# Kernel tuning notes

Hardware: AMD Instinct MI355X
Metric: run time of the kernel (lower is better)

## Reference

```python
import jax, jax.numpy as jnp
import numpy as np

B, T, I, H = 1024, 2048, 2, 64


def setup_inputs() -> dict:
    key = jax.random.key(0)
    k1, k2, k3 = jax.random.split(key, 3)
    x = jax.random.normal(k1, (B, T, I), dtype=jnp.float32)
    # Linear weights, torch nn.Linear layout: [out_features, in_features]
    W_h = jax.random.normal(k2, (H, H), dtype=jnp.float32) * (1.0 / np.sqrt(H))
    W_x = jax.random.normal(k3, (H, I), dtype=jnp.float32) * (1.0 / np.sqrt(I))
    return {"x": x, "W_h": W_h, "W_x": W_x}


def reference(x, W_h, W_x):
    # Manual ReLU RNN: h_{t} = relu(h_{t-1} @ W_h^T + x_t @ W_x^T), h_{-1} = 0
    Bx = x.shape[0]
    Hd = W_h.shape[0]
    h0 = jnp.zeros((Bx, Hd), dtype=x.dtype)
    # Precompute all input projections in one GEMM: [T, B, H]
    xin = jnp.einsum('bti,hi->tbh', x, W_x)

    def step(h, xt):
        h = jax.nn.relu(h @ W_h.T + xt)
        return h, None

    hT, _ = jax.lax.scan(step, h0, xin)
    # outputnn=False, hidden_size>1 -> L2 norm of final hidden state over hidden dim
    return jnp.linalg.norm(hT, axis=-1)  # [B]
```

## Files before the change

kernel.cpp:

```cpp
#include <hip/hip_runtime.h>
#include <math.h>

#define BB 1024
#define TT 2048
#define II 2
#define HH 64

#define PKF(A0,A1,B0,B1,W0,W1) \
 "v_pk_fma_f32 v[" A0 ":" A1 "], v[" B0 ":" B1 "], v[" W0 ":" W1 "], v[" A0 ":" A1 "]\n\t"
#define PKM(A0,A1,B0,B1,W0,W1) \
 "v_pk_mul_f32 v[" A0 ":" A1 "], v[" B0 ":" B1 "], v[" W0 ":" W1 "]\n\t"

#define RD16 \
 "ds_read_b128 v[128:131], v88\n\t" \
 "ds_read_b128 v[132:135], v88 offset:16\n\t" \
 "ds_read_b128 v[136:139], v88 offset:32\n\t" \
 "ds_read_b128 v[140:143], v88 offset:48\n\t" \
 "ds_read_b128 v[144:147], v88 offset:64\n\t" \
 "ds_read_b128 v[148:151], v88 offset:80\n\t" \
 "ds_read_b128 v[152:155], v88 offset:96\n\t" \
 "ds_read_b128 v[156:159], v88 offset:112\n\t" \
 "ds_read_b128 v[160:163], v88 offset:128\n\t" \
 "ds_read_b128 v[164:167], v88 offset:144\n\t" \
 "ds_read_b128 v[168:171], v88 offset:160\n\t" \
 "ds_read_b128 v[172:175], v88 offset:176\n\t" \
 "ds_read_b128 v[176:179], v88 offset:192\n\t" \
 "ds_read_b128 v[180:183], v88 offset:208\n\t" \
 "ds_read_b128 v[184:187], v88 offset:224\n\t" \
 "ds_read_b128 v[188:191], v88 offset:240\n\t"

#define PK_0_7 \
 "v_pk_fma_f32 v[76:77], v[128:129], v[12:13], v[92:93]\n\t" \
 PKM("78","79","130","131","14","15") \
 PKM("80","81","132","133","16","17") \
 PKM("82","83","134","135","18","19") \
 PKF("76","77","136","137","20","21") \
 PKF("78","79","138","139","22","23") \
 PKF("80","81","140","141","24","25") \
 PKF("82","83","142","143","26","27")
#define PK_8_15 \
 PKF("76","77","144","145","28","29") \
 PKF("78","79","146","147","30","31") \
 PKF("80","81","148","149","32","33") \
 PKF("82","83","150","151","34","35") \
 PKF("76","77","152","153","36","37") \
 PKF("78","79","154","155","38","39") \
 PKF("80","81","156","157","40","41") \
 PKF("82","83","158","159","42","43")
#define PK_16_23 \
 PKF("76","77","160","161","44","45") \
 PKF("78","79","162","163","46","47") \
 PKF("80","81","164","165","48","49") \
 PKF("82","83","166","167","50","51") \
 PKF("76","77","168","169","52","53") \
 PKF("78","79","170","171","54","55") \
 PKF("80","81","172","173","56","57") \
 PKF("82","83","174","175","58","59")
#define PK_24_31 \
 PKF("76","77","176","177","60","61") \
 PKF("78","79","178","179","62","63") \
 PKF("80","81","180","181","64","65") \
 PKF("82","83","182","183","66","67") \
 PKF("76","77","184","185","68","69") \
 PKF("78","79","186","187","70","71") \
 PKF("80","81","188","189","72","73") \
 PKF("82","83","190","191","74","75")

#define TAIL \
 "v_pk_add_f32 v[76:77], v[76:77], v[78:79]\n\t" \
 "v_pk_add_f32 v[80:81], v[80:81], v[82:83]\n\t" \
 "v_pk_add_f32 v[76:77], v[76:77], v[80:81]\n\t" \
 "v_add_f32 v84, v76, v77\n\t" \
 "v_max_f32 v84, 0, v84\n\t"

#define BODY(XL, XH, BUMP, LOADX) \
 "ds_write_b32 v86, v84\n\t" \
 RD16 \
 "s_waitcnt vmcnt(1)\n\t" \
 "v_mul_f32 v92, " XL ", v90\n\t" \
 "v_fmac_f32 v92, " XH ", v91\n\t" \
 BUMP \
 LOADX \
 "s_waitcnt lgkmcnt(12)\n\t" \
 PK_0_7 \
 "s_waitcnt lgkmcnt(8)\n\t" \
 PK_8_15 \
 "s_waitcnt lgkmcnt(4)\n\t" \
 PK_16_23 \
 "s_waitcnt lgkmcnt(0)\n\t" \
 PK_24_31 \
 TAIL

#define BUMP_EVEN \
 "v_add_u32 v100, 16, v100\n\t" \
 "v_min_u32 v100, 0x3ff0, v100\n\t"
#define LOAD_EVEN "global_load_dwordx2 v[96:97], v100, %[xb]\n\t"
#define LOAD_ODD  "global_load_dwordx2 v[98:99], v100, %[xb] offset:8\n\t"

__global__ __launch_bounds__(64, 1) void rnn_scan_kernel(
    const float* __restrict__ x,
    const float* __restrict__ Wh,
    const float* __restrict__ Wx,
    float* __restrict__ out)
{
    extern __shared__ float lds[];

    const int b = blockIdx.x;
    const int j = threadIdx.x;

    const float* xb = x + (size_t)b * TT * II;

    float h;
    asm volatile(
        "v_lshlrev_b32 v101, 8, %[lane]\n\t"
        "global_load_dwordx4 v[12:15], v101, %[wh]\n\t"
        "global_load_dwordx4 v[16:19], v101, %[wh] offset:16\n\t"
        "global_load_dwordx4 v[20:23], v101, %[wh] offset:32\n\t"
        "global_load_dwordx4 v[24:27], v101, %[wh] offset:48\n\t"
        "global_load_dwordx4 v[28:31], v101, %[wh] offset:64\n\t"
        "global_load_dwordx4 v[32:35], v101, %[wh] offset:80\n\t"
        "global_load_dwordx4 v[36:39], v101, %[wh] offset:96\n\t"
        "global_load_dwordx4 v[40:43], v101, %[wh] offset:112\n\t"
        "global_load_dwordx4 v[44:47], v101, %[wh] offset:128\n\t"
        "global_load_dwordx4 v[48:51], v101, %[wh] offset:144\n\t"
        "global_load_dwordx4 v[52:55], v101, %[wh] offset:160\n\t"
        "global_load_dwordx4 v[56:59], v101, %[wh] offset:176\n\t"
        "global_load_dwordx4 v[60:63], v101, %[wh] offset:192\n\t"
        "global_load_dwordx4 v[64:67], v101, %[wh] offset:208\n\t"
        "global_load_dwordx4 v[68:71], v101, %[wh] offset:224\n\t"
        "global_load_dwordx4 v[72:75], v101, %[wh] offset:240\n\t"
        "v_lshlrev_b32 v102, 3, %[lane]\n\t"
        "global_load_dwordx2 v[90:91], v102, %[wx]\n\t"
        "v_mov_b32 v100, 0\n\t"
        "global_load_dwordx2 v[96:97], v100, %[xb]\n\t"
        "global_load_dwordx2 v[98:99], v100, %[xb] offset:8\n\t"
        "v_lshlrev_b32 v86, 2, %[lane]\n\t"
        "v_mov_b32 v88, 0\n\t"
        "v_mov_b32 v84, 0\n\t"
        "v_mov_b32 v93, 0\n\t"
        "s_movk_i32 s16, 0x400\n\t"
        "s_waitcnt vmcnt(2)\n\t"
        "LTOP_%=:\n\t"
        BODY("v96", "v97", BUMP_EVEN, LOAD_EVEN)
        BODY("v98", "v99", , LOAD_ODD)
        "s_sub_u32 s16, s16, 1\n\t"
        "s_cmp_lg_u32 s16, 0\n\t"
        "s_cbranch_scc1 LTOP_%=\n\t"
        "s_waitcnt vmcnt(0) lgkmcnt(0)\n\t"
        "v_mov_b32 %[h], v84\n\t"
        : [h] "=&v"(h)
        : [lane] "v"(j), [wh] "s"(Wh), [xb] "s"(xb), [wx] "s"(Wx)
        : "memory", "scc",
          "v12","v13","v14","v15","v16","v17","v18","v19",
          "v20","v21","v22","v23","v24","v25","v26","v27",
          "v28","v29","v30","v31","v32","v33","v34","v35",
          "v36","v37","v38","v39","v40","v41","v42","v43",
          "v44","v45","v46","v47","v48","v49","v50","v51",
          "v52","v53","v54","v55","v56","v57","v58","v59",
          "v60","v61","v62","v63","v64","v65","v66","v67",
          "v68","v69","v70","v71","v72","v73","v74","v75",
          "v76","v77","v78","v79","v80","v81","v82","v83",
          "v84","v86","v88","v90","v91","v92","v93",
          "v96","v97","v98","v99","v100","v101","v102",
          "v128","v129","v130","v131","v132","v133","v134","v135",
          "v136","v137","v138","v139","v140","v141","v142","v143",
          "v144","v145","v146","v147","v148","v149","v150","v151",
          "v152","v153","v154","v155","v156","v157","v158","v159",
          "v160","v161","v162","v163","v164","v165","v166","v167",
          "v168","v169","v170","v171","v172","v173","v174","v175",
          "v176","v177","v178","v179","v180","v181","v182","v183",
          "v184","v185","v186","v187","v188","v189","v190","v191",
          "s16");

    float s = h * h;
#pragma unroll
    for (int off = 32; off > 0; off >>= 1)
        s += __shfl_xor(s, off, 64);
    if (j == 0)
        out[b] = sqrtf(s);
}

extern "C" void kernel_launch(void* const* d_in, const int* in_sizes, int n_in,
                              void* d_out, int out_size, void* d_ws, size_t ws_size,
                              hipStream_t stream) {
    const float* x  = (const float*)d_in[0];
    const float* Wh = (const float*)d_in[1];
    const float* Wx = (const float*)d_in[2];
    float* out = (float*)d_out;

    rnn_scan_kernel<<<dim3(BB), dim3(64), 256, stream>>>(x, Wh, Wx, out);
}
```

Baseline: 303.3 us.

## Split hidden-state exchange between DPP broadcasts and LDS reads in RNN step

Half of the 64-wide matrix-vector product per timestep now takes h values straight from registers. It uses v_permlane16_swap plus row_newbcast DPP modifiers on v_fmac/v_mul, so those terms need no LDS round trip. The other half still reads h from LDS, but only 8 ds_read_b128 per step instead of 16. W_h is loaded into registers in a permuted layout to match. The goal is to shorten the serial per-step latency on the recurrence's critical path, at the cost of 32 scalar DPP FMAs replacing 16 packed FMAs and a more fragile lane mapping.

```diff
diff --git a/kernel.cpp b/kernel.cpp
--- a/kernel.cpp
+++ b/kernel.cpp
@@ -6,12 +6,21 @@
 #define II 2
 #define HH 64
 
-#define PKF(A0,A1,B0,B1,W0,W1) \
- "v_pk_fma_f32 v[" A0 ":" A1 "], v[" B0 ":" B1 "], v[" W0 ":" W1 "], v[" A0 ":" A1 "]\n\t"
-#define PKM(A0,A1,B0,B1,W0,W1) \
- "v_pk_mul_f32 v[" A0 ":" A1 "], v[" B0 ":" B1 "], v[" W0 ":" W1 "]\n\t"
+#define FM(a,c,w,r) "v_fmac_f32 " a ", " c ", " w " row_newbcast:" r "\n\t"
+#define MU(a,c,w,r) "v_mul_f32 "  a ", " c ", " w " row_newbcast:" r "\n\t"
 
-#define RD16 \
+#define QA \
+ MU("v76","v80","v12","0")  MU("v77","v80","v13","1")  MU("v78","v80","v14","2")  MU("v79","v80","v15","3") \
+ FM("v76","v80","v16","4")  FM("v77","v80","v17","5")  FM("v78","v80","v18","6")  FM("v79","v80","v19","7") \
+ FM("v76","v80","v20","8")  FM("v77","v80","v21","9")  FM("v78","v80","v22","10") FM("v79","v80","v23","11") \
+ FM("v76","v80","v24","12") FM("v77","v80","v25","13") FM("v78","v80","v26","14") FM("v79","v80","v27","15")
+#define QB \
+ FM("v76","v81","v28","0")  FM("v77","v81","v29","1")  FM("v78","v81","v30","2")  FM("v79","v81","v31","3") \
+ FM("v76","v81","v32","4")  FM("v77","v81","v33","5")  FM("v78","v81","v34","6")  FM("v79","v81","v35","7") \
+ FM("v76","v81","v36","8")  FM("v77","v81","v37","9")  FM("v78","v81","v38","10") FM("v79","v81","v39","11") \
+ FM("v76","v81","v40","12") FM("v77","v81","v41","13") FM("v78","v81","v42","14") FM("v79","v81","v43","15")
+
+#define RD8 \
  "ds_read_b128 v[128:131], v88\n\t" \
  "ds_read_b128 v[132:135], v88 offset:16\n\t" \
  "ds_read_b128 v[136:139], v88 offset:32\n\t" \
@@ -19,76 +28,53 @@
  "ds_read_b128 v[144:147], v88 offset:64\n\t" \
  "ds_read_b128 v[148:151], v88 offset:80\n\t" \
  "ds_read_b128 v[152:155], v88 offset:96\n\t" \
- "ds_read_b128 v[156:159], v88 offset:112\n\t" \
- "ds_read_b128 v[160:163], v88 offset:128\n\t" \
- "ds_read_b128 v[164:167], v88 offset:144\n\t" \
- "ds_read_b128 v[168:171], v88 offset:160\n\t" \
- "ds_read_b128 v[172:175], v88 offset:176\n\t" \
- "ds_read_b128 v[176:179], v88 offset:192\n\t" \
- "ds_read_b128 v[180:183], v88 offset:208\n\t" \
- "ds_read_b128 v[184:187], v88 offset:224\n\t" \
- "ds_read_b128 v[188:191], v88 offset:240\n\t"
+ "ds_read_b128 v[156:159], v88 offset:112\n\t"
 
-#define PK_0_7 \
- "v_pk_fma_f32 v[76:77], v[128:129], v[12:13], v[92:93]\n\t" \
- PKM("78","79","130","131","14","15") \
- PKM("80","81","132","133","16","17") \
- PKM("82","83","134","135","18","19") \
- PKF("76","77","136","137","20","21") \
- PKF("78","79","138","139","22","23") \
- PKF("80","81","140","141","24","25") \
- PKF("82","83","142","143","26","27")
-#define PK_8_15 \
- PKF("76","77","144","145","28","29") \
- PKF("78","79","146","147","30","31") \
- PKF("80","81","148","149","32","33") \
- PKF("82","83","150","151","34","35") \
- PKF("76","77","152","153","36","37") \
- PKF("78","79","154","155","38","39") \
- PKF("80","81","156","157","40","41") \
- PKF("82","83","158","159","42","43")
-#define PK_16_23 \
- PKF("76","77","160","161","44","45") \
- PKF("78","79","162","163","46","47") \
- PKF("80","81","164","165","48","49") \
- PKF("82","83","166","167","50","51") \
- PKF("76","77","168","169","52","53") \
- PKF("78","79","170","171","54","55") \
- PKF("80","81","172","173","56","57") \
- PKF("82","83","174","175","58","59")
-#define PK_24_31 \
- PKF("76","77","176","177","60","61") \
- PKF("78","79","178","179","62","63") \
- PKF("80","81","180","181","64","65") \
- PKF("82","83","182","183","66","67") \
- PKF("76","77","184","185","68","69") \
- PKF("78","79","186","187","70","71") \
- PKF("80","81","188","189","72","73") \
- PKF("82","83","190","191","74","75")
+#define PK_A \
+ "v_pk_fma_f32 v[104:105], v[128:129], v[44:45], v[92:93]\n\t" \
+ "v_pk_mul_f32 v[106:107], v[130:131], v[46:47]\n\t" \
+ "v_pk_fma_f32 v[104:105], v[132:133], v[48:49], v[104:105]\n\t" \
+ "v_pk_fma_f32 v[106:107], v[134:135], v[50:51], v[106:107]\n\t" \
+ "v_pk_fma_f32 v[104:105], v[136:137], v[52:53], v[104:105]\n\t" \
+ "v_pk_fma_f32 v[106:107], v[138:139], v[54:55], v[106:107]\n\t" \
+ "v_pk_fma_f32 v[104:105], v[140:141], v[56:57], v[104:105]\n\t" \
+ "v_pk_fma_f32 v[106:107], v[142:143], v[58:59], v[106:107]\n\t"
+#define PK_B \
+ "v_pk_fma_f32 v[104:105], v[144:145], v[60:61], v[104:105]\n\t" \
+ "v_pk_fma_f32 v[106:107], v[146:147], v[62:63], v[106:107]\n\t" \
+ "v_pk_fma_f32 v[104:105], v[148:149], v[64:65], v[104:105]\n\t" \
+ "v_pk_fma_f32 v[106:107], v[150:151], v[66:67], v[106:107]\n\t" \
+ "v_pk_fma_f32 v[104:105], v[152:153], v[68:69], v[104:105]\n\t" \
+ "v_pk_fma_f32 v[106:107], v[154:155], v[70:71], v[106:107]\n\t" \
+ "v_pk_fma_f32 v[104:105], v[156:157], v[72:73], v[104:105]\n\t" \
+ "v_pk_fma_f32 v[106:107], v[158:159], v[74:75], v[106:107]\n\t"
 
 #define TAIL \
- "v_pk_add_f32 v[76:77], v[76:77], v[78:79]\n\t" \
- "v_pk_add_f32 v[80:81], v[80:81], v[82:83]\n\t" \
- "v_pk_add_f32 v[76:77], v[76:77], v[80:81]\n\t" \
- "v_add_f32 v84, v76, v77\n\t" \
- "v_max_f32 v84, 0, v84\n\t"
+ "v_pk_add_f32 v[104:105], v[104:105], v[106:107]\n\t" \
+ "v_add_f32 v104, v104, v105\n\t" \
+ "v_add_f32 v76, v76, v77\n\t" \
+ "v_add_f32 v78, v78, v79\n\t" \
+ "v_add_f32 v76, v76, v78\n\t" \
+ "v_add_f32 v76, v76, v104\n\t" \
+ "v_max_f32 v84, 0, v76\n\t" \
+ "v_max_f32 v80, 0, v76\n\t" \
+ "v_max_f32 v81, 0, v76\n\t"
 
 #define BODY(XL, XH, BUMP, LOADX) \
  "ds_write_b32 v86, v84\n\t" \
- RD16 \
+ RD8 \
+ "v_permlane16_swap_b32 v80, v81\n\t" \
  "s_waitcnt vmcnt(1)\n\t" \
  "v_mul_f32 v92, " XL ", v90\n\t" \
  "v_fmac_f32 v92, " XH ", v91\n\t" \
  BUMP \
  LOADX \
- "s_waitcnt lgkmcnt(12)\n\t" \
- PK_0_7 \
- "s_waitcnt lgkmcnt(8)\n\t" \
- PK_8_15 \
+ QA \
+ QB \
  "s_waitcnt lgkmcnt(4)\n\t" \
- PK_16_23 \
+ PK_A \
  "s_waitcnt lgkmcnt(0)\n\t" \
- PK_24_31 \
+ PK_B \
  TAIL
 
 #define BUMP_EVEN \
@@ -112,31 +98,47 @@
 
     float h;
     asm volatile(
+        "v_mov_b32 v80, %[lane]\n\t"
+        "v_mov_b32 v81, %[lane]\n\t"
+        "s_nop 7\n\t"
+        "v_permlane16_swap_b32 v80, v81\n\t"
+        "s_nop 7\n\t"
+        "v_lshrrev_b32 v102, 4, v80\n\t"
+        "v_lshlrev_b32 v102, 6, v102\n\t"
+        "v_lshrrev_b32 v103, 4, v81\n\t"
+        "v_lshlrev_b32 v103, 6, v103\n\t"
         "v_lshlrev_b32 v101, 8, %[lane]\n\t"
-        "global_load_dwordx4 v[12:15], v101, %[wh]\n\t"
-        "global_load_dwordx4 v[16:19], v101, %[wh] offset:16\n\t"
-        "global_load_dwordx4 v[20:23], v101, %[wh] offset:32\n\t"
-        "global_load_dwordx4 v[24:27], v101, %[wh] offset:48\n\t"
-        "global_load_dwordx4 v[28:31], v101, %[wh] offset:64\n\t"
-        "global_load_dwordx4 v[32:35], v101, %[wh] offset:80\n\t"
-        "global_load_dwordx4 v[36:39], v101, %[wh] offset:96\n\t"
-        "global_load_dwordx4 v[40:43], v101, %[wh] offset:112\n\t"
-        "global_load_dwordx4 v[44:47], v101, %[wh] offset:128\n\t"
-        "global_load_dwordx4 v[48:51], v101, %[wh] offset:144\n\t"
-        "global_load_dwordx4 v[52:55], v101, %[wh] offset:160\n\t"
-        "global_load_dwordx4 v[56:59], v101, %[wh] offset:176\n\t"
-        "global_load_dwordx4 v[60:63], v101, %[wh] offset:192\n\t"
-        "global_load_dwordx4 v[64:67], v101, %[wh] offset:208\n\t"
-        "global_load_dwordx4 v[68:71], v101, %[wh] offset:224\n\t"
-        "global_load_dwordx4 v[72:75], v101, %[wh] offset:240\n\t"
+        "v_add_u32 v102, v101, v102\n\t"
+        "v_add_u32 v103, v101, v103\n\t"
+        "global_load_dwordx4 v[12:15], v102, %[wh]\n\t"
+        "global_load_dwordx4 v[16:19], v102, %[wh] offset:16\n\t"
+        "global_load_dwordx4 v[20:23], v102, %[wh] offset:32\n\t"
+        "global_load_dwordx4 v[24:27], v102, %[wh] offset:48\n\t"
+        "global_load_dwordx4 v[28:31], v103, %[wh]\n\t"
+        "global_load_dwordx4 v[32:35], v103, %[wh] offset:16\n\t"
+        "global_load_dwordx4 v[36:39], v103, %[wh] offset:32\n\t"
+        "global_load_dwordx4 v[40:43], v103, %[wh] offset:48\n\t"
+        "v_lshrrev_b32 v88, 5, %[lane]\n\t"
+        "v_xor_b32 v88, 1, v88\n\t"
+        "v_lshlrev_b32 v88, 7, v88\n\t"
+        "v_add_u32 v103, v101, v88\n\t"
+        "global_load_dwordx4 v[44:47], v103, %[wh]\n\t"
+        "global_load_dwordx4 v[48:51], v103, %[wh] offset:16\n\t"
+        "global_load_dwordx4 v[52:55], v103, %[wh] offset:32\n\t"
+        "global_load_dwordx4 v[56:59], v103, %[wh] offset:48\n\t"
+        "global_load_dwordx4 v[60:63], v103, %[wh] offset:64\n\t"
+        "global_load_dwordx4 v[64:67], v103, %[wh] offset:80\n\t"
+        "global_load_dwordx4 v[68:71], v103, %[wh] offset:96\n\t"
+        "global_load_dwordx4 v[72:75], v103, %[wh] offset:112\n\t"
         "v_lshlrev_b32 v102, 3, %[lane]\n\t"
         "global_load_dwordx2 v[90:91], v102, %[wx]\n\t"
         "v_mov_b32 v100, 0\n\t"
         "global_load_dwordx2 v[96:97], v100, %[xb]\n\t"
         "global_load_dwordx2 v[98:99], v100, %[xb] offset:8\n\t"
         "v_lshlrev_b32 v86, 2, %[lane]\n\t"
-        "v_mov_b32 v88, 0\n\t"
         "v_mov_b32 v84, 0\n\t"
+        "v_mov_b32 v80, 0\n\t"
+        "v_mov_b32 v81, 0\n\t"
         "v_mov_b32 v93, 0\n\t"
         "s_movk_i32 s16, 0x400\n\t"
         "s_waitcnt vmcnt(2)\n\t"
@@ -159,17 +161,13 @@
           "v52","v53","v54","v55","v56","v57","v58","v59",
           "v60","v61","v62","v63","v64","v65","v66","v67",
           "v68","v69","v70","v71","v72","v73","v74","v75",
-          "v76","v77","v78","v79","v80","v81","v82","v83",
-          "v84","v86","v88","v90","v91","v92","v93",
-          "v96","v97","v98","v99","v100","v101","v102",
+          "v76","v77","v78","v79","v80","v81","v84","v86","v88",
+          "v90","v91","v92","v93","v96","v97","v98","v99",
+          "v100","v101","v102","v103","v104","v105","v106","v107",
           "v128","v129","v130","v131","v132","v133","v134","v135",
           "v136","v137","v138","v139","v140","v141","v142","v143",
           "v144","v145","v146","v147","v148","v149","v150","v151",
           "v152","v153","v154","v155","v156","v157","v158","v159",
-          "v160","v161","v162","v163","v164","v165","v166","v167",
-          "v168","v169","v170","v171","v172","v173","v174","v175",
-          "v176","v177","v178","v179","v180","v181","v182","v183",
-          "v184","v185","v186","v187","v188","v189","v190","v191",
           "s16");
 
     float s = h * h;
```

Result: slower. 334.5 us (+10.3%).

## Compute a quarter of the recurrence via DPP row broadcast instead of LDS reads

Applied to the files above, without the earlier changes.

Each lane now takes 16 of the 64 hidden-state products directly from the h register, using DPP row_newbcast to broadcast values within each 16-lane row. Only the remaining 48 values come from LDS, which is now double-written and read at a per-row rotated offset, so each step issues 12 LDS reads instead of 16. The W_h row is loaded in a matching rotated order. The goal is to cut LDS read traffic and latency on the serial per-timestep critical path, at the cost of more complex addressing and a dependence on DPP broadcast semantics.

```diff
diff --git a/kernel.cpp b/kernel.cpp
--- a/kernel.cpp
+++ b/kernel.cpp
@@ -6,12 +6,16 @@
 #define II 2
 #define HH 64
 
-#define PKF(A0,A1,B0,B1,W0,W1) \
- "v_pk_fma_f32 v[" A0 ":" A1 "], v[" B0 ":" B1 "], v[" W0 ":" W1 "], v[" A0 ":" A1 "]\n\t"
-#define PKM(A0,A1,B0,B1,W0,W1) \
- "v_pk_mul_f32 v[" A0 ":" A1 "], v[" B0 ":" B1 "], v[" W0 ":" W1 "]\n\t"
+#define FM(a,w,r) "v_fmac_f32 " a ", v84, " w " row_newbcast:" r "\n\t"
+#define MU(a,w,r) "v_mul_f32 "  a ", v84, " w " row_newbcast:" r "\n\t"
 
-#define RD16 \
+#define Q0 \
+ MU("v78","v12","0")  MU("v79","v13","1")  FM("v78","v14","2")  FM("v79","v15","3") \
+ FM("v78","v16","4")  FM("v79","v17","5")  FM("v78","v18","6")  FM("v79","v19","7") \
+ FM("v78","v20","8")  FM("v79","v21","9")  FM("v78","v22","10") FM("v79","v23","11") \
+ FM("v78","v24","12") FM("v79","v25","13") FM("v78","v26","14") FM("v79","v27","15")
+
+#define RD12 \
  "ds_read_b128 v[128:131], v88\n\t" \
  "ds_read_b128 v[132:135], v88 offset:16\n\t" \
  "ds_read_b128 v[136:139], v88 offset:32\n\t" \
@@ -23,72 +27,61 @@
  "ds_read_b128 v[160:163], v88 offset:128\n\t" \
  "ds_read_b128 v[164:167], v88 offset:144\n\t" \
  "ds_read_b128 v[168:171], v88 offset:160\n\t" \
- "ds_read_b128 v[172:175], v88 offset:176\n\t" \
- "ds_read_b128 v[176:179], v88 offset:192\n\t" \
- "ds_read_b128 v[180:183], v88 offset:208\n\t" \
- "ds_read_b128 v[184:187], v88 offset:224\n\t" \
- "ds_read_b128 v[188:191], v88 offset:240\n\t"
+ "ds_read_b128 v[172:175], v88 offset:176\n\t"
 
 #define PK_0_7 \
- "v_pk_fma_f32 v[76:77], v[128:129], v[12:13], v[92:93]\n\t" \
- PKM("78","79","130","131","14","15") \
- PKM("80","81","132","133","16","17") \
- PKM("82","83","134","135","18","19") \
- PKF("76","77","136","137","20","21") \
- PKF("78","79","138","139","22","23") \
- PKF("80","81","140","141","24","25") \
- PKF("82","83","142","143","26","27")
+ "v_pk_fma_f32 v[104:105], v[128:129], v[28:29], v[92:93]\n\t" \
+ "v_pk_mul_f32 v[106:107], v[130:131], v[30:31]\n\t" \
+ "v_pk_mul_f32 v[108:109], v[132:133], v[32:33]\n\t" \
+ "v_pk_mul_f32 v[110:111], v[134:135], v[34:35]\n\t" \
+ "v_pk_fma_f32 v[104:105], v[136:137], v[36:37], v[104:105]\n\t" \
+ "v_pk_fma_f32 v[106:107], v[138:139], v[38:39], v[106:107]\n\t" \
+ "v_pk_fma_f32 v[108:109], v[140:141], v[40:41], v[108:109]\n\t" \
+ "v_pk_fma_f32 v[110:111], v[142:143], v[42:43], v[110:111]\n\t"
 #define PK_8_15 \
- PKF("76","77","144","145","28","29") \
- PKF("78","79","146","147","30","31") \
- PKF("80","81","148","149","32","33") \
- PKF("82","83","150","151","34","35") \
- PKF("76","77","152","153","36","37") \
- PKF("78","79","154","155","38","39") \
- PKF("80","81","156","157","40","41") \
- PKF("82","83","158","159","42","43")
+ "v_pk_fma_f32 v[104:105], v[144:145], v[44:45], v[104:105]\n\t" \
+ "v_pk_fma_f32 v[106:107], v[146:147], v[46:47], v[106:107]\n\t" \
+ "v_pk_fma_f32 v[108:109], v[148:149], v[48:49], v[108:109]\n\t" \
+ "v_pk_fma_f32 v[110:111], v[150:151], v[50:51], v[110:111]\n\t" \
+ "v_pk_fma_f32 v[104:105], v[152:153], v[52:53], v[104:105]\n\t" \
+ "v_pk_fma_f32 v[106:107], v[154:155], v[54:55], v[106:107]\n\t" \
+ "v_pk_fma_f32 v[108:109], v[156:157], v[56:57], v[108:109]\n\t" \
+ "v_pk_fma_f32 v[110:111], v[158:159], v[58:59], v[110:111]\n\t"
 #define PK_16_23 \
- PKF("76","77","160","161","44","45") \
- PKF("78","79","162","163","46","47") \
- PKF("80","81","164","165","48","49") \
- PKF("82","83","166","167","50","51") \
- PKF("76","77","168","169","52","53") \
- PKF("78","79","170","171","54","55") \
- PKF("80","81","172","173","56","57") \
- PKF("82","83","174","175","58","59")
-#define PK_24_31 \
- PKF("76","77","176","177","60","61") \
- PKF("78","79","178","179","62","63") \
- PKF("80","81","180","181","64","65") \
- PKF("82","83","182","183","66","67") \
- PKF("76","77","184","185","68","69") \
- PKF("78","79","186","187","70","71") \
- PKF("80","81","188","189","72","73") \
- PKF("82","83","190","191","74","75")
+ "v_pk_fma_f32 v[104:105], v[160:161], v[60:61], v[104:105]\n\t" \
+ "v_pk_fma_f32 v[106:107], v[162:163], v[62:63], v[106:107]\n\t" \
+ "v_pk_fma_f32 v[108:109], v[164:165], v[64:65], v[108:109]\n\t" \
+ "v_pk_fma_f32 v[110:111], v[166:167], v[66:67], v[110:111]\n\t" \
+ "v_pk_fma_f32 v[104:105], v[168:169], v[68:69], v[104:105]\n\t" \
+ "v_pk_fma_f32 v[106:107], v[170:171], v[70:71], v[106:107]\n\t" \
+ "v_pk_fma_f32 v[108:109], v[172:173], v[72:73], v[108:109]\n\t" \
+ "v_pk_fma_f32 v[110:111], v[174:175], v[74:75], v[110:111]\n\t"
 
 #define TAIL \
- "v_pk_add_f32 v[76:77], v[76:77], v[78:79]\n\t" \
- "v_pk_add_f32 v[80:81], v[80:81], v[82:83]\n\t" \
- "v_pk_add_f32 v[76:77], v[76:77], v[80:81]\n\t" \
- "v_add_f32 v84, v76, v77\n\t" \
- "v_max_f32 v84, 0, v84\n\t"
+ "v_pk_add_f32 v[104:105], v[104:105], v[106:107]\n\t" \
+ "v_pk_add_f32 v[108:109], v[108:109], v[110:111]\n\t" \
+ "v_pk_add_f32 v[104:105], v[104:105], v[108:109]\n\t" \
+ "v_add_f32 v104, v104, v105\n\t" \
+ "v_add_f32 v78, v78, v79\n\t" \
+ "v_add_f32 v104, v104, v78\n\t" \
+ "v_max_f32 v84, 0, v104\n\t"
 
 #define BODY(XL, XH, BUMP, LOADX) \
  "ds_write_b32 v86, v84\n\t" \
- RD16 \
+ "ds_write_b32 v86, v84 offset:256\n\t" \
+ RD12 \
  "s_waitcnt vmcnt(1)\n\t" \
  "v_mul_f32 v92, " XL ", v90\n\t" \
  "v_fmac_f32 v92, " XH ", v91\n\t" \
  BUMP \
  LOADX \
- "s_waitcnt lgkmcnt(12)\n\t" \
+ Q0 \
+ "s_waitcnt lgkmcnt(8)\n\t" \
  PK_0_7 \
- "s_waitcnt lgkmcnt(8)\n\t" \
+ "s_waitcnt lgkmcnt(4)\n\t" \
  PK_8_15 \
- "s_waitcnt lgkmcnt(4)\n\t" \
+ "s_waitcnt lgkmcnt(0)\n\t" \
  PK_16_23 \
- "s_waitcnt lgkmcnt(0)\n\t" \
- PK_24_31 \
  TAIL
 
 #define BUMP_EVEN \
@@ -96,6 +89,12 @@
  "v_min_u32 v100, 0x3ff0, v100\n\t"
 #define LOAD_EVEN "global_load_dwordx2 v[96:97], v100, %[xb]\n\t"
 #define LOAD_ODD  "global_load_dwordx2 v[98:99], v100, %[xb] offset:8\n\t"
+
+#define PKW(i, d0, d3) \
+ "v_add_u32 v106, " #i ", v88\n\t" \
+ "v_and_b32 v106, 0xff, v106\n\t" \
+ "v_add_u32 v106, v101, v106\n\t" \
+ "global_load_dwordx4 v[" #d0 ":" #d3 "], v106, %[wh]\n\t"
 
 __global__ __launch_bounds__(64, 1) void rnn_scan_kernel(
     const float* __restrict__ x,
@@ -113,29 +112,32 @@
     float h;
     asm volatile(
         "v_lshlrev_b32 v101, 8, %[lane]\n\t"
-        "global_load_dwordx4 v[12:15], v101, %[wh]\n\t"
-        "global_load_dwordx4 v[16:19], v101, %[wh] offset:16\n\t"
-        "global_load_dwordx4 v[20:23], v101, %[wh] offset:32\n\t"
-        "global_load_dwordx4 v[24:27], v101, %[wh] offset:48\n\t"
-        "global_load_dwordx4 v[28:31], v101, %[wh] offset:64\n\t"
-        "global_load_dwordx4 v[32:35], v101, %[wh] offset:80\n\t"
-        "global_load_dwordx4 v[36:39], v101, %[wh] offset:96\n\t"
-        "global_load_dwordx4 v[40:43], v101, %[wh] offset:112\n\t"
-        "global_load_dwordx4 v[44:47], v101, %[wh] offset:128\n\t"
-        "global_load_dwordx4 v[48:51], v101, %[wh] offset:144\n\t"
-        "global_load_dwordx4 v[52:55], v101, %[wh] offset:160\n\t"
-        "global_load_dwordx4 v[56:59], v101, %[wh] offset:176\n\t"
-        "global_load_dwordx4 v[60:63], v101, %[wh] offset:192\n\t"
-        "global_load_dwordx4 v[64:67], v101, %[wh] offset:208\n\t"
-        "global_load_dwordx4 v[68:71], v101, %[wh] offset:224\n\t"
-        "global_load_dwordx4 v[72:75], v101, %[wh] offset:240\n\t"
-        "v_lshlrev_b32 v102, 3, %[lane]\n\t"
-        "global_load_dwordx2 v[90:91], v102, %[wx]\n\t"
+        "v_lshrrev_b32 v102, 4, %[lane]\n\t"
+        "v_lshlrev_b32 v103, 6, v102\n\t"
+        "v_add_u32 v104, v101, v103\n\t"
+        "global_load_dwordx4 v[12:15], v104, %[wh]\n\t"
+        "global_load_dwordx4 v[16:19], v104, %[wh] offset:16\n\t"
+        "global_load_dwordx4 v[20:23], v104, %[wh] offset:32\n\t"
+        "global_load_dwordx4 v[24:27], v104, %[wh] offset:48\n\t"
+        "v_add_u32 v88, 64, v103\n\t"
+        PKW(0,   28, 31)
+        PKW(16,  32, 35)
+        PKW(32,  36, 39)
+        PKW(48,  40, 43)
+        PKW(64,  44, 47)
+        PKW(80,  48, 51)
+        PKW(96,  52, 55)
+        PKW(112, 56, 59)
+        PKW(128, 60, 63)
+        PKW(144, 64, 67)
+        PKW(160, 68, 71)
+        PKW(176, 72, 75)
+        "v_lshlrev_b32 v105, 3, %[lane]\n\t"
+        "global_load_dwordx2 v[90:91], v105, %[wx]\n\t"
         "v_mov_b32 v100, 0\n\t"
         "global_load_dwordx2 v[96:97], v100, %[xb]\n\t"
         "global_load_dwordx2 v[98:99], v100, %[xb] offset:8\n\t"
         "v_lshlrev_b32 v86, 2, %[lane]\n\t"
-        "v_mov_b32 v88, 0\n\t"
         "v_mov_b32 v84, 0\n\t"
         "v_mov_b32 v93, 0\n\t"
         "s_movk_i32 s16, 0x400\n\t"
@@ -159,17 +161,16 @@
           "v52","v53","v54","v55","v56","v57","v58","v59",
           "v60","v61","v62","v63","v64","v65","v66","v67",
           "v68","v69","v70","v71","v72","v73","v74","v75",
-          "v76","v77","v78","v79","v80","v81","v82","v83",
-          "v84","v86","v88","v90","v91","v92","v93",
-          "v96","v97","v98","v99","v100","v101","v102",
+          "v78","v79","v84","v86","v88",
+          "v90","v91","v92","v93","v96","v97","v98","v99",
+          "v100","v101","v102","v103","v104","v105","v106","v107",
+          "v108","v109","v110","v111",
           "v128","v129","v130","v131","v132","v133","v134","v135",
           "v136","v137","v138","v139","v140","v141","v142","v143",
           "v144","v145","v146","v147","v148","v149","v150","v151",
           "v152","v153","v154","v155","v156","v157","v158","v159",
           "v160","v161","v162","v163","v164","v165","v166","v167",
           "v168","v169","v170","v171","v172","v173","v174","v175",
-          "v176","v177","v178","v179","v180","v181","v182","v183",
-          "v184","v185","v186","v187","v188","v189","v190","v191",
           "s16");
 
     float s = h * h;
@@ -188,5 +189,5 @@
     const float* Wx = (const float*)d_in[2];
     float* out = (float*)d_out;
 
-    rnn_scan_kernel<<<dim3(BB), dim3(64), 256, stream>>>(x, Wh, Wx, out);
+    rnn_scan_kernel<<<dim3(BB), dim3(64), 512, stream>>>(x, Wh, Wx, out);
 }
```

Result: slower. 315.4 us (+4.0%).
